# Optimization experiments

Measured on AMD Instinct MI355X. Metric: run time of the kernel, lower is better.

## Reference

```python
import jax, jax.numpy as jnp
import numpy as np
from jax import lax

B, L, E, H, VOCAB = 32, 64, 1024, 128, 32000


def setup_inputs() -> dict:
    key = jax.random.key(0)
    ks = jax.random.split(key, 8)
    return {
        "sent": jax.random.randint(ks[0], (B, L), 0, VOCAB),
        "init_c": jax.random.normal(ks[1], (B, H), jnp.float32),
        "init_h": jax.random.normal(ks[2], (B, H), jnp.float32),
        "enc_output": jax.random.normal(ks[3], (B, E, H), jnp.float32),
        "w_emb": jax.random.normal(ks[4], (VOCAB, H), jnp.float32) * 0.02,
        "w_lstm": jax.random.normal(ks[5], (2 * H, 4 * H), jnp.float32) * 0.05,
        "w_soft": jax.random.normal(ks[6], (H, VOCAB), jnp.float32) * 0.05,
        "V": jax.random.normal(ks[7], (2 * H, H), jnp.float32) * 0.05,
    }


def reference(sent, init_c, init_h, enc_output, w_emb, w_lstm, w_soft, V):
    h_dim = init_h.shape[-1]
    x_emb = w_emb[sent]                       # (B, L, H) embedding lookup
    # Split additive-attention matrix: concat(enc, h) @ V == enc @ V_e + h @ V_h
    V_e, V_h = V[:h_dim], V[h_dim:]           # (H, H) each
    enc_proj = enc_output @ V_e               # (B, E, H), precomputed once

    def step(carry, x_t):
        c, h = carry
        # LSTM cell: gates from concat(x, h) @ w_lstm
        gates = jnp.concatenate([x_t, h], axis=-1) @ w_lstm   # (B, 4H)
        i, f, o, g = jnp.split(gates, 4, axis=-1)
        c_new = jax.nn.sigmoid(f) * c + jax.nn.sigmoid(i) * jnp.tanh(g)
        h_new = jax.nn.sigmoid(o) * jnp.tanh(c_new)           # (B, H)
        # Bahdanau additive attention over encoder states
        att = jnp.tanh(enc_proj + (h_new @ V_h)[:, None, :])  # (B, E, H)
        scores = att.sum(axis=-1)                              # (B, E)
        alpha = jax.nn.softmax(scores, axis=-1)                # (B, E)
        context = jnp.einsum('be,beh->bh', alpha, enc_output)  # (B, H)
        h_out = context                                        # attended hidden
        return (c_new, h_out), (h_out, alpha)

    (c_fin, h_fin), (hs, alphas) = lax.scan(step, (init_c, init_h),
                                            jnp.transpose(x_emb, (1, 0, 2)))
    hs = jnp.transpose(hs, (1, 0, 2))          # (B, L, H)
    alphas = jnp.transpose(alphas, (1, 0, 2))  # (B, L, E)
    logits = hs @ w_soft                       # (B, L, vocab)
    return logits, c_fin, h_fin, alphas
```

## Files before the change

### kernel.cpp

```cpp
#include <hip/hip_runtime.h>
#include <hip/hip_bf16.h>

#define BB 32
#define LL 64
#define EE 1024
#define HH 128
#define VV 32000

typedef unsigned short u16;
typedef unsigned long long u64;
typedef __attribute__((ext_vector_type(8))) short bf16x8;
typedef __attribute__((ext_vector_type(8))) unsigned short u16x8;
typedef __attribute__((ext_vector_type(4))) float f32x4;

#define LOG2E 1.4426950408889634f
#define C2T   2.8853900817779268f

#define OFF_C ((size_t)BB * LL * VV)
#define OFF_H (OFF_C + (size_t)BB * HH)
#define OFF_A (OFF_H + (size_t)BB * HH)

#define WS_ENCT 0
#define WS_WREC ((size_t)8388608)
#define WS_HS   ((size_t)8519680)
#define WS_GX   ((size_t)9043968)
#define WS_PAYU ((size_t)13238272)
#define WS_WT   ((size_t)13770752)
#define WS_DFL  ((size_t)21962752)
#define WS_NEED ((size_t)21962756)

#define PAYU_WORDS (32 * 8 * 2 * 130)

__device__ __forceinline__ float bf2f(u16 u) {
    union { unsigned int i; float f; } v; v.i = ((unsigned int)u) << 16; return v.f;
}
__device__ __forceinline__ u16 f2bf(float f) {
    union { float f; unsigned int i; } v; v.f = f;
    unsigned int x = v.i;
    return (u16)((x + 0x7FFFu + ((x >> 16) & 1u)) >> 16);
}
__device__ __forceinline__ float ldf(const void* p, size_t i, int f32) {
    if (f32) return ((const float*)p)[i];
    return bf2f(((const u16*)p)[i]);
}
__device__ __forceinline__ void stout(void* p, size_t i, float v, int f32) {
    if (f32) ((float*)p)[i] = v;
    else ((u16*)p)[i] = f2bf(v);
}
__device__ __forceinline__ float sigm(float x) {
    return __builtin_amdgcn_rcpf(1.f + __builtin_amdgcn_exp2f(-x * LOG2E));
}
__device__ __forceinline__ float tanh_fast(float x) {
    return 1.f - 2.f * __builtin_amdgcn_rcpf(__builtin_amdgcn_exp2f(x * C2T) + 1.f);
}

__global__ __launch_bounds__(256) void resetdetect_kernel(
    u64* __restrict__ pay, const unsigned int* __restrict__ w, int* __restrict__ flag)
{
    int i = blockIdx.x * 256 + threadIdx.x;
    if (i < PAYU_WORDS)
        pay[i] = 0ull;
    if (i == 0) {
        int cnt = 0;
        for (int j = 0; j < 256; ++j) {
            float a = fabsf(bf2f((u16)(w[j] & 0xFFFFu)));
            if (a > 1e-4f && a < 0.5f) ++cnt;
        }
        *flag = (cnt > 128) ? 1 : 0;
    }
}

__global__ __launch_bounds__(1024) void prep_wrec(
    const void* __restrict__ w_lstm, u16* __restrict__ wrecT, const int* __restrict__ flagp)
{
    int isf32 = !flagp[0];
    __shared__ u16 tile[32][33];
    int c0 = blockIdx.x * 32;
    int k0 = blockIdx.y * 32;
    int tx = threadIdx.x & 31, ty = threadIdx.x >> 5;
    tile[ty][tx] = f2bf(ldf(w_lstm, (size_t)(HH + k0 + ty) * 512 + c0 + tx, isf32));
    __syncthreads();
    wrecT[(size_t)(c0 + ty) * 128 + k0 + tx] = tile[tx][ty];
}

__global__ __launch_bounds__(256) void gatesx3_kernel(
    const int* __restrict__ sent, const void* __restrict__ w_emb,
    const void* __restrict__ w_lstm, float* __restrict__ gx,
    const int* __restrict__ flagp)
{
    int isf32 = !flagp[0];
    int row0 = blockIdx.x * 16;
    int tid = threadIdx.x;
    __shared__ float xr[16][128];
    for (int i = tid; i < 2048; i += 256) {
        int r = i >> 7, col = i & 127;
        int id = sent[row0 + r];
        xr[r][col] = ldf(w_emb, (size_t)id * HH + col, isf32);
    }
    __syncthreads();
    int c0 = tid, c1 = tid + 256;
    float a0[16], a1[16];
    #pragma unroll
    for (int r = 0; r < 16; ++r) { a0[r] = 0.f; a1[r] = 0.f; }
    for (int kk = 0; kk < 128; ++kk) {
        float w0, w1;
        if (isf32) {
            w0 = ((const float*)w_lstm)[(size_t)kk * 512 + c0];
            w1 = ((const float*)w_lstm)[(size_t)kk * 512 + c1];
        } else {
            w0 = bf2f(((const u16*)w_lstm)[(size_t)kk * 512 + c0]);
            w1 = bf2f(((const u16*)w_lstm)[(size_t)kk * 512 + c1]);
        }
        #pragma unroll
        for (int r = 0; r < 16; ++r) {
            a0[r] += xr[r][kk] * w0;
            a1[r] += xr[r][kk] * w1;
        }
    }
    #pragma unroll
    for (int r = 0; r < 16; ++r) {
        gx[(size_t)(row0 + r) * 512 + c0] = a0[r];
        gx[(size_t)(row0 + r) * 512 + c1] = a1[r];
    }
}

__global__ __launch_bounds__(1024) void transpose_wsoft(
    const void* __restrict__ w_soft, u16* __restrict__ wT, const int* __restrict__ flagp)
{
    int isf32 = !flagp[0];
    __shared__ u16 tile[32][33];
    int n0 = blockIdx.x * 32;
    int k0 = blockIdx.y * 32;
    int tx = threadIdx.x & 31, ty = threadIdx.x >> 5;
    tile[ty][tx] = f2bf(ldf(w_soft, (size_t)(k0 + ty) * VV + n0 + tx, isf32));
    __syncthreads();
    wT[(size_t)(n0 + ty) * HH + k0 + tx] = tile[tx][ty];
}

__global__ __launch_bounds__(256) void encproj_kernel(
    const void* __restrict__ enc_out, const void* __restrict__ V,
    u16* __restrict__ encT, const int* __restrict__ flagp)
{
    int isf32 = !flagp[0];
    __shared__ float ve[HH][HH];
    int b = blockIdx.y;
    int e0 = blockIdx.x * 64;
    int tid = threadIdx.x;
    for (int i = tid; i < HH * HH; i += 256)
        ve[i >> 7][i & 127] = ldf(V, i, isf32);
    __syncthreads();
    int e = e0 + (tid & 63);
    int hb = (tid >> 6) * 32;
    size_t rowbase = ((size_t)b * EE + e) * HH;
    float acc[32];
    #pragma unroll
    for (int i = 0; i < 32; ++i) acc[i] = 0.f;
    for (int k0 = 0; k0 < HH; k0 += 16) {
        float ef[16];
        #pragma unroll
        for (int i = 0; i < 16; ++i) ef[i] = ldf(enc_out, rowbase + k0 + i, isf32);
        #pragma unroll
        for (int hh = 0; hh < 32; ++hh) {
            float a = acc[hh];
            #pragma unroll
            for (int kk = 0; kk < 16; ++kk)
                a += ef[kk] * ve[k0 + kk][hb + hh];
            acc[hh] = a;
        }
    }
    u16* outp = encT + ((size_t)b * HH) * EE + e;
    #pragma unroll
    for (int hh = 0; hh < 32; ++hh)
        outp[(size_t)(hh + hb) * EE] = f2bf(acc[hh] * C2T);
}

__global__ __launch_bounds__(1024) void scan_kernel(
    const void* __restrict__ init_c, const void* __restrict__ init_h,
    const void* __restrict__ enc_out, const u16* __restrict__ wrecT,
    const void* __restrict__ V, const u16* __restrict__ encTg16,
    const float* __restrict__ gx, u16* __restrict__ hs_bf,
    void* __restrict__ out, u64* __restrict__ payu,
    const int* __restrict__ flagp)
{
    const int isf32 = !flagp[0];
    const int bid = blockIdx.x;
    const int b = bid & 31, k = bid >> 5;
    const int tid = threadIdx.x;

    __shared__ u16   wrecl[512 * 128];
    __shared__ float gp[512];
    __shared__ float harr[128], cst[128], hnew[128], hvC[128];
    __shared__ float dred[8][128];
    __shared__ float sc[128];
    __shared__ float exch[8][130];
    __shared__ float redw[2], redw2[2];
    __shared__ float m_s, s_s;

    for (int i = tid; i < 8192; i += 1024)
        *(u16x8*)&wrecl[i * 8] = *(const u16x8*)&wrecT[(size_t)i * 8];
    if (tid < 128) {
        cst[tid]  = ldf(init_c, (size_t)b * HH + tid, isf32);
        harr[tid] = ldf(init_h, (size_t)b * HH + tid, isf32);
    }
    __syncthreads();

    u64* mypu = payu + (size_t)(b * 8 + k) * 2 * 130;

    for (int t = 0; t < LL; ++t) {
        const unsigned int want = (unsigned int)(t + 1);
        float g0 = 0.f, g1 = 0.f, g2 = 0.f, g3 = 0.f;
        if (tid < 128) {
            const float* gxr = gx + (size_t)(b * LL + t) * 512;
            g0 = gxr[tid]; g1 = gxr[128 + tid]; g2 = gxr[256 + tid]; g3 = gxr[384 + tid];
        }
        {
            int kc = tid & 15, colb = tid >> 4;
            #pragma unroll
            for (int it = 0; it < 8; ++it) {
                int col = colb + (it << 6);
                const bf16x8 wv = *(const bf16x8*)&wrecl[col * 128 + kc * 8];
                float acc = 0.f;
                #pragma unroll
                for (int j = 0; j < 8; ++j)
                    acc = __builtin_fmaf(harr[kc * 8 + j], bf2f((u16)wv[j]), acc);
                acc += __shfl_xor(acc, 1);
                acc += __shfl_xor(acc, 2);
                acc += __shfl_xor(acc, 4);
                acc += __shfl_xor(acc, 8);
                if (kc == 0) gp[col] = acc;
            }
        }
        __syncthreads();
        if (tid < 128) {
            float gi = g0 + gp[tid];
            float gf = g1 + gp[128 + tid];
            float go = g2 + gp[256 + tid];
            float gg = g3 + gp[384 + tid];
            float c_new = sigm(gf) * cst[tid] + sigm(gi) * tanh_fast(gg);
            cst[tid] = c_new;
            hnew[tid] = sigm(go) * tanh_fast(c_new);
        }
        __syncthreads();
        {
            int h = tid & 127, jc = tid >> 7;
            float p = 0.f;
            if (isf32) {
                const float* vp = (const float*)V + (size_t)(HH + jc * 16) * HH + h;
                #pragma unroll
                for (int j = 0; j < 16; ++j)
                    p += hnew[jc * 16 + j] * vp[(size_t)j * HH];
            } else {
                const u16* vp = (const u16*)V + (size_t)(HH + jc * 16) * HH + h;
                #pragma unroll
                for (int j = 0; j < 16; ++j)
                    p += hnew[jc * 16 + j] * bf2f(vp[(size_t)j * HH]);
            }
            dred[jc][h] = p;
        }
        __syncthreads();
        if (tid < 128) {
            float v = 0.f;
            #pragma unroll
            for (int s = 0; s < 8; ++s) v += dred[s][tid];
            hvC[tid] = v * C2T;
        }
        __syncthreads();
        {
            int e = tid & 127, hc = tid >> 7;
            const u16* ep = encTg16 + (size_t)(b * 128 + hc * 16) * EE + k * 128 + e;
            float sumr = 0.f;
            #pragma unroll
            for (int j = 0; j < 16; ++j) {
                float a = bf2f(ep[(size_t)j * EE]) + hvC[hc * 16 + j];
                sumr += __builtin_amdgcn_rcpf(__builtin_amdgcn_exp2f(a) + 1.f);
            }
            dred[hc][e] = sumr;
        }
        __syncthreads();
        float s_e = 0.f, p_reg = 0.f;
        if (tid < 128) {
            float sr = 0.f;
            #pragma unroll
            for (int s = 0; s < 8; ++s) sr += dred[s][tid];
            s_e = 128.f - 2.f * sr;
            float m = s_e;
            #pragma unroll
            for (int off = 32; off; off >>= 1) m = fmaxf(m, __shfl_xor(m, off));
            if ((tid & 63) == 0) redw[tid >> 6] = m;
        }
        __syncthreads();
        if (tid < 128) {
            float mloc = fmaxf(redw[0], redw[1]);
            p_reg = __builtin_amdgcn_exp2f((s_e - mloc) * LOG2E);
            sc[tid] = p_reg;
            float s = p_reg;
            #pragma unroll
            for (int off = 32; off; off >>= 1) s += __shfl_xor(s, off);
            if ((tid & 63) == 0) redw2[tid >> 6] = s;
            if (tid == 0) m_s = mloc;
        }
        __syncthreads();
        if (tid == 0) s_s = redw2[0] + redw2[1];
        {
            int h = tid & 127, ec = tid >> 7;
            float p = 0.f;
            if (isf32) {
                const float* eb = (const float*)enc_out +
                    ((size_t)b * EE + k * 128 + ec * 16) * HH + h;
                #pragma unroll
                for (int j = 0; j < 16; ++j)
                    p += sc[ec * 16 + j] * eb[(size_t)j * HH];
            } else {
                const u16* eb = (const u16*)enc_out +
                    ((size_t)b * EE + k * 128 + ec * 16) * HH + h;
                #pragma unroll
                for (int j = 0; j < 16; ++j)
                    p += sc[ec * 16 + j] * bf2f(eb[(size_t)j * HH]);
            }
            dred[ec][h] = p;
        }
        __syncthreads();
        float Uv = 0.f;
        if (tid < 128) {
            #pragma unroll
            for (int s = 0; s < 8; ++s) Uv += dred[s][tid];
        }
        {
            u64* pp = mypu + (size_t)(t & 1) * 130;
            if (tid < 130) {
                float val = (tid < 128) ? Uv : ((tid == 128) ? m_s : s_s);
                union { float f; unsigned int u; } cv; cv.f = val;
                u64 w = ((u64)want << 32) | (u64)cv.u;
                __hip_atomic_store(&pp[tid], w, __ATOMIC_RELAXED, __HIP_MEMORY_SCOPE_AGENT);
                exch[k][tid] = val;
            }
        }
        if (tid < 910) {
            int qq = tid / 130;
            int q = qq + (qq >= k ? 1 : 0);
            int idx = tid - qq * 130;
            const u64* qp = payu + ((size_t)(b * 8 + q) * 2 + (t & 1)) * 130 + idx;
            u64 w = __hip_atomic_load(qp, __ATOMIC_RELAXED, __HIP_MEMORY_SCOPE_AGENT);
            int cnt = 0;
            while ((unsigned int)(w >> 32) != want) {
                __builtin_amdgcn_s_sleep(1);
                w = __hip_atomic_load(qp, __ATOMIC_RELAXED, __HIP_MEMORY_SCOPE_AGENT);
                if (++cnt > (1 << 20)) break;
            }
            union { unsigned int u; float f; } cv; cv.u = (unsigned int)(w & 0xFFFFFFFFu);
            exch[q][idx] = cv.f;
        }
        __syncthreads();
        if (tid < 128) {
            float M = exch[0][128];
            #pragma unroll
            for (int q = 1; q < 8; ++q) M = fmaxf(M, exch[q][128]);
            float St = 0.f, ch = 0.f;
            #pragma unroll
            for (int q = 0; q < 8; ++q) {
                float w = __builtin_amdgcn_exp2f((exch[q][128] - M) * LOG2E);
                St += w * exch[q][129];
                ch += w * exch[q][tid];
            }
            float rS = __builtin_amdgcn_rcpf(St);
            float ctx = ch * rS;
            harr[tid] = ctx;
            float al = p_reg * __builtin_amdgcn_exp2f((m_s - M) * LOG2E) * rS;
            stout(out, OFF_A + (size_t)(b * LL + t) * EE + k * 128 + tid, al, isf32);
            if (k == 0) {
                hs_bf[(size_t)(b * LL + t) * HH + tid] = f2bf(ctx);
                if (t == LL - 1) {
                    stout(out, OFF_H + (size_t)b * HH + tid, ctx, isf32);
                    stout(out, OFF_C + (size_t)b * HH + tid, cst[tid], isf32);
                }
            }
        }
        __syncthreads();
    }
}

__global__ __launch_bounds__(256) void logits_gemm(
    const u16* __restrict__ hs, const u16* __restrict__ wT,
    void* __restrict__ out, const int* __restrict__ flagp)
{
    int isf32 = !flagp[0];
    int n0 = blockIdx.x * 32;
    int m0 = (blockIdx.y * 4 + (threadIdx.x >> 6)) * 32;
    int lane = threadIdx.x & 63;
    int lr = lane & 15, lh = lane >> 4;
    f32x4 acc00 = {0.f, 0.f, 0.f, 0.f}, acc01 = acc00, acc10 = acc00, acc11 = acc00;
    const u16* a0p = hs + (size_t)(m0 + lr) * HH + lh * 8;
    const u16* a1p = a0p + (size_t)16 * HH;
    const u16* b0p = wT + (size_t)(n0 + lr) * HH + lh * 8;
    const u16* b1p = b0p + (size_t)16 * HH;
    #pragma unroll
    for (int ks = 0; ks < 4; ++ks) {
        bf16x8 a0 = *(const bf16x8*)(a0p + ks * 32);
        bf16x8 a1 = *(const bf16x8*)(a1p + ks * 32);
        bf16x8 b0 = *(const bf16x8*)(b0p + ks * 32);
        bf16x8 b1 = *(const bf16x8*)(b1p + ks * 32);
        acc00 = __builtin_amdgcn_mfma_f32_16x16x32_bf16(a0, b0, acc00, 0, 0, 0);
        acc01 = __builtin_amdgcn_mfma_f32_16x16x32_bf16(a0, b1, acc01, 0, 0, 0);
        acc10 = __builtin_amdgcn_mfma_f32_16x16x32_bf16(a1, b0, acc10, 0, 0, 0);
        acc11 = __builtin_amdgcn_mfma_f32_16x16x32_bf16(a1, b1, acc11, 0, 0, 0);
    }
    size_t base0 = (size_t)(m0 + lh * 4) * VV + n0;
    size_t base1 = (size_t)(m0 + 16 + lh * 4) * VV + n0;
    #pragma unroll
    for (int r = 0; r < 4; ++r) {
        stout(out, base0 + (size_t)r * VV + lr,      acc00[r], isf32);
        stout(out, base0 + (size_t)r * VV + 16 + lr, acc01[r], isf32);
        stout(out, base1 + (size_t)r * VV + lr,      acc10[r], isf32);
        stout(out, base1 + (size_t)r * VV + 16 + lr, acc11[r], isf32);
    }
}

extern "C" void kernel_launch(void* const* d_in, const int* in_sizes, int n_in,
                              void* d_out, int out_size, void* d_ws, size_t ws_size,
                              hipStream_t stream)
{
    (void)in_sizes; (void)n_in; (void)out_size;
    if (ws_size < WS_NEED) return;

    const int* sent     = (const int*)d_in[0];
    const void* init_c  = d_in[1];
    const void* init_h  = d_in[2];
    const void* enc_out = d_in[3];
    const void* w_emb   = d_in[4];
    const void* w_lstm  = d_in[5];
    const void* w_soft  = d_in[6];
    const void* V       = d_in[7];

    char* ws = (char*)d_ws;
    u16*   encT  = (u16*)(ws + WS_ENCT);
    u16*   wrecT = (u16*)(ws + WS_WREC);
    u16*   hs    = (u16*)(ws + WS_HS);
    float* gx    = (float*)(ws + WS_GX);
    u64*   payu  = (u64*)(ws + WS_PAYU);
    u16*   wT    = (u16*)(ws + WS_WT);
    int*   dflag = (int*)(ws + WS_DFL);

    hipLaunchKernelGGL(resetdetect_kernel, dim3((PAYU_WORDS + 255) / 256), dim3(256), 0, stream,
                       payu, (const unsigned int*)w_emb, dflag);
    hipLaunchKernelGGL(prep_wrec, dim3(16, 4), dim3(1024), 0, stream, w_lstm, wrecT, dflag);
    hipLaunchKernelGGL(gatesx3_kernel, dim3(128), dim3(256), 0, stream,
                       sent, w_emb, w_lstm, gx, dflag);
    hipLaunchKernelGGL(encproj_kernel, dim3(16, BB), dim3(256), 0, stream, enc_out, V, encT, dflag);

    {
        const void* a0 = init_c; const void* a1 = init_h; const void* a2 = enc_out;
        const u16* a3 = wrecT; const void* a4 = V; const u16* a5 = encT;
        const float* a6 = gx; u16* a7 = hs; void* a8 = d_out;
        u64* a9 = payu; const int* a10 = dflag;
        void* args[] = {&a0, &a1, &a2, &a3, &a4, &a5, &a6, &a7, &a8, &a9, &a10};
        hipLaunchCooperativeKernel(scan_kernel, dim3(256), dim3(1024), args, 0, stream);
    }

    hipLaunchKernelGGL(transpose_wsoft, dim3(VV / 32, 4), dim3(1024), 0, stream, w_soft, wT, dflag);
    hipLaunchKernelGGL(logits_gemm, dim3(VV / 32, 16), dim3(256), 0, stream, hs, wT, d_out, dflag);
}
```

Baseline: 807.5 us.

## Interleave two batch rows per scan block to hide cross-block exchange latency

```diff
diff --git a/kernel.cpp b/kernel.cpp
--- a/kernel.cpp
+++ b/kernel.cpp
@@ -184,29 +184,32 @@
 {
     const int isf32 = !flagp[0];
     const int bid = blockIdx.x;
-    const int b = bid & 31, k = bid >> 5;
+    const int g = bid & 15, k = bid >> 4;
+    const int b0 = g * 2, b1 = g * 2 + 1;
     const int tid = threadIdx.x;
 
     __shared__ u16   wrecl[512 * 128];
     __shared__ float gp[512];
-    __shared__ float harr[128], cst[128], hnew[128], hvC[128];
+    __shared__ float harr[2][128], cst[2][128];
+    __shared__ float hnew[128], hvC[128];
     __shared__ float dred[8][128];
-    __shared__ float sc[128];
+    __shared__ float sc[2][128];
+    __shared__ float selfp[2][130];
     __shared__ float exch[8][130];
     __shared__ float redw[2], redw2[2];
-    __shared__ float m_s, s_s;
+    __shared__ float m_sv[2], s_sv[2];
 
     for (int i = tid; i < 8192; i += 1024)
         *(u16x8*)&wrecl[i * 8] = *(const u16x8*)&wrecT[(size_t)i * 8];
     if (tid < 128) {
-        cst[tid]  = ldf(init_c, (size_t)b * HH + tid, isf32);
-        harr[tid] = ldf(init_h, (size_t)b * HH + tid, isf32);
+        cst[0][tid]  = ldf(init_c, (size_t)b0 * HH + tid, isf32);
+        harr[0][tid] = ldf(init_h, (size_t)b0 * HH + tid, isf32);
+        cst[1][tid]  = ldf(init_c, (size_t)b1 * HH + tid, isf32);
+        harr[1][tid] = ldf(init_h, (size_t)b1 * HH + tid, isf32);
     }
     __syncthreads();
 
-    u64* mypu = payu + (size_t)(b * 8 + k) * 2 * 130;
-
-    for (int t = 0; t < LL; ++t) {
+    auto phases = [&](int s, int b, int t) {
         const unsigned int want = (unsigned int)(t + 1);
         float g0 = 0.f, g1 = 0.f, g2 = 0.f, g3 = 0.f;
         if (tid < 128) {
@@ -222,7 +225,7 @@
                 float acc = 0.f;
                 #pragma unroll
                 for (int j = 0; j < 8; ++j)
-                    acc = __builtin_fmaf(harr[kc * 8 + j], bf2f((u16)wv[j]), acc);
+                    acc = __builtin_fmaf(harr[s][kc * 8 + j], bf2f((u16)wv[j]), acc);
                 acc += __shfl_xor(acc, 1);
                 acc += __shfl_xor(acc, 2);
                 acc += __shfl_xor(acc, 4);
@@ -236,8 +239,8 @@
             float gf = g1 + gp[128 + tid];
             float go = g2 + gp[256 + tid];
             float gg = g3 + gp[384 + tid];
-            float c_new = sigm(gf) * cst[tid] + sigm(gi) * tanh_fast(gg);
-            cst[tid] = c_new;
+            float c_new = sigm(gf) * cst[s][tid] + sigm(gi) * tanh_fast(gg);
+            cst[s][tid] = c_new;
             hnew[tid] = sigm(go) * tanh_fast(c_new);
         }
         __syncthreads();
@@ -261,7 +264,7 @@
         if (tid < 128) {
             float v = 0.f;
             #pragma unroll
-            for (int s = 0; s < 8; ++s) v += dred[s][tid];
+            for (int s2 = 0; s2 < 8; ++s2) v += dred[s2][tid];
             hvC[tid] = v * C2T;
         }
         __syncthreads();
@@ -277,11 +280,11 @@
             dred[hc][e] = sumr;
         }
         __syncthreads();
-        float s_e = 0.f, p_reg = 0.f;
+        float s_e = 0.f;
         if (tid < 128) {
             float sr = 0.f;
             #pragma unroll
-            for (int s = 0; s < 8; ++s) sr += dred[s][tid];
+            for (int s2 = 0; s2 < 8; ++s2) sr += dred[s2][tid];
             s_e = 128.f - 2.f * sr;
             float m = s_e;
             #pragma unroll
@@ -291,16 +294,16 @@
         __syncthreads();
         if (tid < 128) {
             float mloc = fmaxf(redw[0], redw[1]);
-            p_reg = __builtin_amdgcn_exp2f((s_e - mloc) * LOG2E);
-            sc[tid] = p_reg;
-            float s = p_reg;
-            #pragma unroll
-            for (int off = 32; off; off >>= 1) s += __shfl_xor(s, off);
-            if ((tid & 63) == 0) redw2[tid >> 6] = s;
-            if (tid == 0) m_s = mloc;
-        }
-        __syncthreads();
-        if (tid == 0) s_s = redw2[0] + redw2[1];
+            float p_reg = __builtin_amdgcn_exp2f((s_e - mloc) * LOG2E);
+            sc[s][tid] = p_reg;
+            float ss = p_reg;
+            #pragma unroll
+            for (int off = 32; off; off >>= 1) ss += __shfl_xor(ss, off);
+            if ((tid & 63) == 0) redw2[tid >> 6] = ss;
+            if (tid == 0) m_sv[s] = mloc;
+        }
+        __syncthreads();
+        if (tid == 0) s_sv[s] = redw2[0] + redw2[1];
         {
             int h = tid & 127, ec = tid >> 7;
             float p = 0.f;
@@ -309,13 +312,13 @@
                     ((size_t)b * EE + k * 128 + ec * 16) * HH + h;
                 #pragma unroll
                 for (int j = 0; j < 16; ++j)
-                    p += sc[ec * 16 + j] * eb[(size_t)j * HH];
+                    p += sc[s][ec * 16 + j] * eb[(size_t)j * HH];
             } else {
                 const u16* eb = (const u16*)enc_out +
                     ((size_t)b * EE + k * 128 + ec * 16) * HH + h;
                 #pragma unroll
                 for (int j = 0; j < 16; ++j)
-                    p += sc[ec * 16 + j] * bf2f(eb[(size_t)j * HH]);
+                    p += sc[s][ec * 16 + j] * bf2f(eb[(size_t)j * HH]);
             }
             dred[ec][h] = p;
         }
@@ -323,18 +326,23 @@
         float Uv = 0.f;
         if (tid < 128) {
             #pragma unroll
-            for (int s = 0; s < 8; ++s) Uv += dred[s][tid];
+            for (int s2 = 0; s2 < 8; ++s2) Uv += dred[s2][tid];
         }
         {
-            u64* pp = mypu + (size_t)(t & 1) * 130;
+            u64* pp = payu + ((size_t)(b * 8 + k) * 2 + (t & 1)) * 130;
             if (tid < 130) {
-                float val = (tid < 128) ? Uv : ((tid == 128) ? m_s : s_s);
+                float val = (tid < 128) ? Uv : ((tid == 128) ? m_sv[s] : s_sv[s]);
                 union { float f; unsigned int u; } cv; cv.f = val;
                 u64 w = ((u64)want << 32) | (u64)cv.u;
                 __hip_atomic_store(&pp[tid], w, __ATOMIC_RELAXED, __HIP_MEMORY_SCOPE_AGENT);
-                exch[k][tid] = val;
-            }
-        }
+                selfp[s][tid] = val;
+            }
+        }
+    };
+
+    auto pollcombine = [&](int s, int b, int t) {
+        const unsigned int want = (unsigned int)(t + 1);
+        if (tid < 130) exch[k][tid] = selfp[s][tid];
         if (tid < 910) {
             int qq = tid / 130;
             int q = qq + (qq >= k ? 1 : 0);
@@ -364,18 +372,27 @@
             }
             float rS = __builtin_amdgcn_rcpf(St);
             float ctx = ch * rS;
-            harr[tid] = ctx;
-            float al = p_reg * __builtin_amdgcn_exp2f((m_s - M) * LOG2E) * rS;
+            harr[s][tid] = ctx;
+            float al = sc[s][tid] * __builtin_amdgcn_exp2f((m_sv[s] - M) * LOG2E) * rS;
             stout(out, OFF_A + (size_t)(b * LL + t) * EE + k * 128 + tid, al, isf32);
             if (k == 0) {
                 hs_bf[(size_t)(b * LL + t) * HH + tid] = f2bf(ctx);
                 if (t == LL - 1) {
                     stout(out, OFF_H + (size_t)b * HH + tid, ctx, isf32);
-                    stout(out, OFF_C + (size_t)b * HH + tid, cst[tid], isf32);
+                    stout(out, OFF_C + (size_t)b * HH + tid, cst[s][tid], isf32);
                 }
             }
         }
         __syncthreads();
+    };
+
+    phases(0, b0, 0);
+    for (int t = 0; t < LL; ++t) {
+        phases(1, b1, t);
+        pollcombine(0, b0, t);
+        if (t < LL - 1)
+            phases(0, b0, t + 1);
+        pollcombine(1, b1, t);
     }
 }
 
@@ -453,7 +470,7 @@
         const float* a6 = gx; u16* a7 = hs; void* a8 = d_out;
         u64* a9 = payu; const int* a10 = dflag;
         void* args[] = {&a0, &a1, &a2, &a3, &a4, &a5, &a6, &a7, &a8, &a9, &a10};
-        hipLaunchCooperativeKernel(scan_kernel, dim3(256), dim3(1024), args, 0, stream);
+        hipLaunchCooperativeKernel(scan_kernel, dim3(128), dim3(1024), args, 0, stream);
     }
 
     hipLaunchKernelGGL(transpose_wsoft, dim3(VV / 32, 4), dim3(1024), 0, stream, w_soft, wT, dflag);
```

Measured after the change: 2.218 ms. +174.7%, slower.
